# Optimization experiments

Measured on AMD Instinct MI355X. Metric: run time of the kernel, lower is better.

Reference implementation:

```python
import jax, jax.numpy as jnp
import numpy as np

FEAT_STRIDE = 16
PRE_N = 3000      # n_test_pre_nms
POST_N = 300      # n_test_post_nms
NMS_IOU = 0.7
MIN_SIZE = 16.0
SCALE = 1.0


def _anchor_base():
    base = 16.0
    ratios = np.array([0.5, 1.0, 2.0])
    scales = np.array([8.0, 16.0, 32.0])
    hs = (base * scales[None, :] * np.sqrt(ratios[:, None])).ravel()
    ws = (base * scales[None, :] * np.sqrt(1.0 / ratios[:, None])).ravel()
    px = py = base / 2.0
    return np.stack([px - ws / 2, py - hs / 2, px + ws / 2, py + hs / 2], axis=1).astype(np.float32)  # (9,4)


def _all_anchors(h, w):
    ab = _anchor_base()                                  # (A,4)
    sy = np.arange(h) * FEAT_STRIDE
    sx = np.arange(w) * FEAT_STRIDE
    yy, xx = np.meshgrid(sy, sx, indexing='ij')          # row-major (y,x) matches NHWC flatten
    shifts = np.stack([xx.ravel(), yy.ravel(), xx.ravel(), yy.ravel()], axis=1).astype(np.float32)
    return jnp.asarray((shifts[:, None, :] + ab[None, :, :]).reshape(-1, 4))  # (h*w*A, 4)


def _loc2box(anchor, loc):
    w = anchor[:, 2] - anchor[:, 0]
    h = anchor[:, 3] - anchor[:, 1]
    cx = anchor[:, 0] + 0.5 * w
    cy = anchor[:, 1] + 0.5 * h
    ctr_x = loc[:, 0] * w + cx
    ctr_y = loc[:, 1] * h + cy
    nw = jnp.exp(loc[:, 2]) * w
    nh = jnp.exp(loc[:, 3]) * h
    return jnp.stack([ctr_x - 0.5 * nw, ctr_y - 0.5 * nh, ctr_x + 0.5 * nw, ctr_y + 0.5 * nh], axis=1)


def _iou(b):
    area = (b[:, 2] - b[:, 0]) * (b[:, 3] - b[:, 1])
    x1 = jnp.maximum(b[:, None, 0], b[None, :, 0])
    y1 = jnp.maximum(b[:, None, 1], b[None, :, 1])
    x2 = jnp.minimum(b[:, None, 2], b[None, :, 2])
    y2 = jnp.minimum(b[:, None, 3], b[None, :, 3])
    inter = jnp.maximum(x2 - x1, 0.0) * jnp.maximum(y2 - y1, 0.0)
    return inter / (area[:, None] + area[None, :] - inter + 1e-9)


def _proposals(loc, score, anchor, img_h, img_w):
    roi = _loc2box(anchor, loc)
    roi = jnp.stack([jnp.clip(roi[:, 0], 0.0, img_w), jnp.clip(roi[:, 1], 0.0, img_h),
                     jnp.clip(roi[:, 2], 0.0, img_w), jnp.clip(roi[:, 3], 0.0, img_h)], axis=1)
    ms = MIN_SIZE * SCALE
    valid = ((roi[:, 2] - roi[:, 0]) >= ms) & ((roi[:, 3] - roi[:, 1]) >= ms)
    score = jnp.where(valid, score, -1e9)  # size filter as masking (jit-friendly)
    _, top_i = jax.lax.top_k(score, PRE_N)  # descending argsort + pre-NMS cut
    boxes = roi[top_i]                       # (PRE_N,4), score-sorted
    iou = _iou(boxes)
    idx = jnp.arange(PRE_N)

    def body(i, keep):
        sup = jnp.any(keep & (iou[i] > NMS_IOU) & (idx < i))
        return keep.at[i].set(~sup)

    keep = jax.lax.fori_loop(0, PRE_N, body, jnp.zeros((PRE_N,), bool))
    sel = jnp.sort(jnp.where(keep, idx, PRE_N))[:POST_N]
    sel = jnp.where(sel >= PRE_N, 0, sel)  # pad with top box (index 0 is always kept)
    return boxes[sel]                       # (POST_N,4)


def setup_inputs() -> dict:
    key = jax.random.key(0)
    ks = jax.random.split(key, 4)
    n, C, M, H, W, A = 4, 512, 512, 64, 64, 9
    x = jax.random.normal(ks[0], (n, C, H, W), jnp.float32)
    w_conv = jax.random.normal(ks[1], (M, C, 3, 3), jnp.float32) * 0.01
    b_conv = jnp.zeros((M,), jnp.float32)
    w_score = jax.random.normal(ks[2], (A * 2, M, 1, 1), jnp.float32) * 0.01
    b_score = jnp.zeros((A * 2,), jnp.float32)
    w_loc = jax.random.normal(ks[3], (A * 4, M, 1, 1), jnp.float32) * 0.01
    b_loc = jnp.zeros((A * 4,), jnp.float32)
    return dict(x=x, w_conv=w_conv, b_conv=b_conv, w_score=w_score, b_score=b_score,
                w_loc=w_loc, b_loc=b_loc, img_h=1024, img_w=1024)


def reference(x, w_conv, b_conv, w_score, b_score, w_loc, b_loc, img_h, img_w):
    n, _, h, w = x.shape
    dn = ('NCHW', 'OIHW', 'NCHW')
    feat = jax.nn.relu(jax.lax.conv_general_dilated(x, w_conv, (1, 1), 'SAME', dimension_numbers=dn)
                       + b_conv[None, :, None, None])
    rpn_locs = jax.lax.conv_general_dilated(feat, w_loc, (1, 1), 'SAME', dimension_numbers=dn) + b_loc[None, :, None, None]
    rpn_locs = rpn_locs.transpose(0, 2, 3, 1).reshape(n, -1, 4)
    rpn_scores = jax.lax.conv_general_dilated(feat, w_score, (1, 1), 'SAME', dimension_numbers=dn) + b_score[None, :, None, None]
    rpn_scores = rpn_scores.transpose(0, 2, 3, 1).reshape(n, -1, 2)
    fg = jax.nn.softmax(rpn_scores, axis=-1)[:, :, 1]  # (n, h*w*A)
    anchor = _all_anchors(h, w)
    rois = jax.vmap(lambda l, s: _proposals(l, s, anchor, float(img_h), float(img_w)))(rpn_locs, fg)
    roi_indices = jnp.repeat(jnp.arange(n, dtype=jnp.float32)[:, None], POST_N, axis=1)
    return rpn_locs, rpn_scores, rois, roi_indices, anchor[None]
```

## Files before the change

kernel.cpp:

```cpp
#include <hip/hip_runtime.h>
#include <cstdint>
#include <cmath>

#define HW 64
#define NPIX 4096
#define CIN 512
#define NANCH 36864
#define PREN 3000
#define POSTN 300
#define ICL 8
#define NSLOT 13

typedef _Float16 h8v __attribute__((ext_vector_type(8)));
typedef float f16v __attribute__((ext_vector_type(16)));

#define AS1 __attribute__((address_space(1)))
#define AS3 __attribute__((address_space(3)))

__device__ __forceinline__ void gl16(const void* g, void* l) {
  __builtin_amdgcn_global_load_lds((const AS1 void*)g, (AS3 void*)l, 16, 0, 0);
}

__device__ __forceinline__ void f16_split(float f, short& h, short& l) {
  _Float16 hh = (_Float16)f;
  float hf = (float)hh;
  _Float16 ll = (_Float16)(f - hf);
  h = __builtin_bit_cast(short, hh);
  l = __builtin_bit_cast(short, ll);
}


__global__ __launch_bounds__(256) void xform_w_kernel(
    const float* __restrict__ w, short* __restrict__ wth,
    short* __restrict__ wtl, unsigned* __restrict__ zp) {
  const int oc = blockIdx.x;
  const int t = threadIdx.x;
  __shared__ float ws_[4608];
  const float* wr = w + (size_t)oc * 4608;
  for (int i = t; i < 4608; i += 256) ws_[i] = wr[i];
  __syncthreads();
  for (int c = t; c < 576; c += 256) {
    int tap = c / 64;
    int g = c - tap * 64;
    int icc = g >> 2;
    int kh = (g >> 1) & 1;
    int lhh = g & 1;
    h8v hv, lv;
    short* hp = (short*)&hv;
    short* lp = (short*)&lv;
#pragma unroll
    for (int j = 0; j < 8; ++j) {
      short hh, ll;
      f16_split(ws_[(g * 8 + j) * 9 + tap] * 128.0f, hh, ll);
      hp[j] = hh; lp[j] = ll;
    }
    long o = (((((long)tap * 16 + icc) * 2 + kh) * 2 + lhh) * 512 + oc) * 8;
    *(h8v*)(wth + o) = hv;
    *(h8v*)(wtl + o) = lv;
  }
  if (oc == 0 && t < 16) zp[t] = 0u;
}

__global__ __launch_bounds__(256) void xform_x_kernel(
    const float* __restrict__ x, short* __restrict__ xth,
    short* __restrict__ xtl) {
  const int yb = blockIdx.x;
  const int n = blockIdx.y;
  const int t = threadIdx.x;
  __shared__ float xs[64 * 65];
  const float* xr = x + ((size_t)n * 512) * 4096 + yb * 64;
  short* oh = xth + ((size_t)n * 4096 + yb * 64) * 512;
  short* ol = xtl + ((size_t)n * 4096 + yb * 64) * 512;
  for (int icb = 0; icb < 8; ++icb) {
    if (icb) __syncthreads();
#pragma unroll
    for (int q = 0; q < 16; ++q) {
      int idx = q * 256 + t;
      int icl = idx >> 6, xc = idx & 63;
      xs[icl * 65 + xc] = xr[(size_t)(icb * 64 + icl) * 4096 + xc];
    }
    __syncthreads();
#pragma unroll
    for (int q = 0; q < 2; ++q) {
      int c = q * 256 + t;
      int xc = c >> 3, icg = c & 7;
      h8v hv, lv;
      short* hp = (short*)&hv;
      short* lp = (short*)&lv;
#pragma unroll
      for (int j = 0; j < 8; ++j) {
        short hh, ll;
        f16_split(xs[(icg * 8 + j) * 65 + xc] * 2048.0f, hh, ll);
        hp[j] = hh; lp[j] = ll;
      }
      size_t o = (size_t)xc * 512 + icb * 64 + icg * 8;
      *(h8v*)(oh + o) = hv;
      *(h8v*)(ol + o) = lv;
    }
  }
}

__global__ __launch_bounds__(256, 2) void conv3_mfma(
    const short* __restrict__ xth, const short* __restrict__ xtl,
    const short* __restrict__ wth, const short* __restrict__ wtl,
    const float* __restrict__ bconv, const char* __restrict__ zpage,
    float* __restrict__ feat2) {
  const int t = threadIdx.x;
  const int lane = t & 63;
  const int wid = __builtin_amdgcn_readfirstlane(t >> 6);
  const int l31 = lane & 31, lh = lane >> 5;
  const int wm = wid >> 1, wn = wid & 1;

  const int bx = blockIdx.x, by = blockIdx.y, n = blockIdx.z;
  const int k8 = bx & 7;
  const int ocb = k8 & 3;
  const int yp = (k8 >> 2) * 16 + (bx >> 3) * 4 + by;
  const int y0 = yp * 2;
  const int ocbase = ocb * 128;

  __shared__ short As[2][2][272 * 32];
  char* const asb = (char*)&As[0][0][0];

  const char* asrc[9]; int adst[9]; int astep[9];
  {
    const char* xs0 = (const char*)xth;
    const char* xs1 = (const char*)xtl;
#pragma unroll
    for (int k = 0; k < 9; ++k) {
      int bq = wid + 4 * k;
      if (bq < 34) {
        int hl = (bq >= 17) ? 1 : 0;
        int blk = bq - hl * 17;
        int e = blk * 16 + (lane >> 2);
        int slot = lane & 3;
        int r = e / 68;
        int cp = e - r * 68;
        int y = y0 - 1 + r;
        int c = cp - 1;
        bool valid = (cp >= 1) && (cp <= 64) && (y >= 0) && (y < 64);
        int ss = slot ^ ((e >> 1) & 3);
        long off = ((((long)n * 64 + y) * 64 + c) * 512 + ss * 8) * 2;
        asrc[k] = valid ? ((hl ? xs1 : xs0) + off) : (const char*)zpage;
        astep[k] = valid ? 64 : 0;
        adst[k] = hl * 17408 + blk * 1024;
      }
    }
  }

  const long lane_b = (long)lh * 4096 + (long)(ocbase + wn * 64 + l31) * 8;

  struct FragB { h8v h[2][2], l[2][2]; };

#define READ_Bg(F, TAP, ICC) do {                                            \
    long sb_ = ((long)(TAP) * 16 + (ICC)) * 16384 + lane_b;                  \
    _Pragma("unroll")                                                        \
    for (int kh_ = 0; kh_ < 2; ++kh_)                                        \
      _Pragma("unroll")                                                      \
      for (int fn_ = 0; fn_ < 2; ++fn_) {                                    \
        long o_ = sb_ + kh_ * 8192 + fn_ * 256;                              \
        (F).h[kh_][fn_] = *(const h8v*)(wth + o_);                           \
        (F).l[kh_][fn_] = *(const h8v*)(wtl + o_);                           \
      }                                                                      \
  } while (0)

#define COMP_AE(AE, TAP) do {                                                 \
    int dy_ = (TAP) / 3, dx_ = (TAP) - dy_ * 3;                               \
    _Pragma("unroll")                                                         \
    for (int fm_ = 0; fm_ < 2; ++fm_) {                                       \
      int e_ = (wm + dy_) * 68 + fm_ * 32 + l31 + dx_;                        \
      (AE)[fm_] = e_ * 64 + ((lh ^ ((e_ >> 1) & 3)) << 4);                    \
    }                                                                         \
  } while (0)

#define TAP_MFMA(BC, AB) do {                                                 \
    _Pragma("unroll")                                                         \
    for (int kh_ = 0; kh_ < 2; ++kh_) {                                       \
      h8v Ah_[2], Al_[2];                                                     \
      _Pragma("unroll")                                                       \
      for (int fm_ = 0; fm_ < 2; ++fm_) {                                     \
        int a0_ = ae[fm_] ^ (kh_ << 5);                                       \
        Ah_[fm_] = *(const h8v*)((AB) + a0_);                                 \
        Al_[fm_] = *(const h8v*)((AB) + 17408 + a0_);                         \
      }                                                                       \
      _Pragma("unroll")                                                       \
      for (int fm_ = 0; fm_ < 2; ++fm_)                                       \
        _Pragma("unroll")                                                     \
        for (int fn_ = 0; fn_ < 2; ++fn_)                                     \
          acc[fm_][fn_] = __builtin_amdgcn_mfma_f32_32x32x16_f16(             \
              Ah_[fm_], (BC).h[kh_][fn_], acc[fm_][fn_], 0, 0, 0);            \
      _Pragma("unroll")                                                       \
      for (int fm_ = 0; fm_ < 2; ++fm_)                                       \
        _Pragma("unroll")                                                     \
        for (int fn_ = 0; fn_ < 2; ++fn_)                                     \
          acc[fm_][fn_] = __builtin_amdgcn_mfma_f32_32x32x16_f16(             \
              Al_[fm_], (BC).h[kh_][fn_], acc[fm_][fn_], 0, 0, 0);            \
      _Pragma("unroll")                                                       \
      for (int fm_ = 0; fm_ < 2; ++fm_)                                       \
        _Pragma("unroll")                                                     \
        for (int fn_ = 0; fn_ < 2; ++fn_)                                     \
          acc[fm_][fn_] = __builtin_amdgcn_mfma_f32_32x32x16_f16(             \
              Ah_[fm_], (BC).l[kh_][fn_], acc[fm_][fn_], 0, 0, 0);            \
    }                                                                         \
  } while (0)

#define STEP_BODY(BC, BN) do {                                                \
    int tapN_ = tap + 1, iccN_ = icc;                                         \
    if (tapN_ == 9) { tapN_ = 0; iccN_ = (icc < 15) ? icc + 1 : 15; }         \
    READ_Bg(BN, tapN_, iccN_);             \
    if (tap == 0 && icc < 15) {            \
      char* ab_ = asb + ((acur ^ 1) * 34816);                                 \
      _Pragma("unroll")                                                       \
      for (int k_ = 0; k_ < 9; ++k_) {                                        \
        int bq_ = wid + 4 * k_;                                               \
        if (bq_ < 34) { asrc[k_] += astep[k_];                                \
                        gl16(asrc[k_], ab_ + adst[k_]); }                     \
      }                                                                       \
    }                                                                         \
    COMP_AE(ae, tap);                                                         \
    { char* abc_ = asb + (acur * 34816);                                      \
      TAP_MFMA(BC, abc_); }                                                   \
    ++tap;                                                                    \
    if (tap == 9) {                                         \
      tap = 0; ++icc;                                                         \
      _Pragma("unroll")                                                       \
      for (int fm_ = 0; fm_ < 2; ++fm_)                                       \
        _Pragma("unroll")                                                     \
        for (int fn_ = 0; fn_ < 2; ++fn_)                                     \
          _Pragma("unroll")                                                   \
          for (int r_ = 0; r_ < 16; ++r_) {                                   \
            S[fm_][fn_][r_] += acc[fm_][fn_][r_];                             \
            acc[fm_][fn_][r_] = 0.f;                                          \
          }                                                                   \
      __syncthreads();                      \
      acur ^= 1;                                                              \
    }                                                                         \
  } while (0)

  f16v acc[2][2];
  f16v S[2][2];
#pragma unroll
  for (int i = 0; i < 2; ++i)
#pragma unroll
    for (int j = 0; j < 2; ++j)
#pragma unroll
      for (int r = 0; r < 16; ++r) { acc[i][j][r] = 0.f; S[i][j][r] = 0.f; }

#pragma unroll
  for (int k = 0; k < 9; ++k) {
    int bq = wid + 4 * k;
    if (bq < 34) gl16(asrc[k], asb + adst[k]);
  }
  FragB B0, B1;
  READ_Bg(B0, 0, 0);
  __syncthreads();
  int ae[2];
  int tap = 0, icc = 0, acur = 0;

  for (int s2 = 0; s2 < 72; ++s2) {
    STEP_BODY(B0, B1);
    STEP_BODY(B1, B0);
  }

#undef READ_Bg
#undef COMP_AE
#undef TAP_MFMA
#undef STEP_BODY

  const float OS = 1.0f / 262144.0f;
  const float* bb = bconv + ocbase + wn * 64;
#pragma unroll
  for (int fn = 0; fn < 2; ++fn) {
    const float bias = bb[fn * 32 + l31];
#pragma unroll
    for (int fm = 0; fm < 2; ++fm) {
      float* op = feat2 + (((long)n * 4096 + (y0 + wm) * 64 + fm * 32) * 512)
                + ocbase + wn * 64 + fn * 32 + l31;
#pragma unroll
      for (int r = 0; r < 16; ++r) {
        int m = (r & 3) + 8 * (r >> 2) + 4 * lh;
        op[(long)m * 512] = fmaxf(S[fm][fn][r] * OS + bias, 0.f);
      }
    }
  }
}

__global__ __launch_bounds__(256) void zero_hist_kernel(unsigned* __restrict__ h) {
  int i = blockIdx.x * 256 + threadIdx.x;
  if (i < 262160) h[i] = 0u;
}

__global__ __launch_bounds__(256) void reshape_w_kernel(
    const float* __restrict__ w, float* __restrict__ w4,
    unsigned* __restrict__ histz) {
  int gid = blockIdx.x * 256 + threadIdx.x;
  if (gid < 262160) histz[gid] = 0;
  if (gid >= 512 * 512 * 9) return;
  int o4  = gid & 3;
  int r   = gid >> 2;
  int tap = r % 9;
  int r2  = r / 9;
  int h   = r2 & 1;
  int r3  = r2 >> 1;
  int ic  = r3 & 511;
  int g   = r3 >> 9;
  int oc  = (g >> 2) * 32 + (g & 3) * 8 + h * 4 + o4;
  w4[gid] = w[((size_t)oc * 512 + ic) * 9 + tap];
}

#define WLOAD(DST, UPTR) do {                                                \
    _Pragma("unroll")                                                        \
    for (int q = 0; q < 36; ++q) (DST)[q] = (UPTR)[q];                       \
  } while (0)

#define CONV_HALF(W, OB) do {                                                \
    _Pragma("unroll")                                                        \
    for (int r = 0; r < 3; ++r)                                              \
    _Pragma("unroll")                                                        \
    for (int kx = 0; kx < 3; ++kx) {                                         \
      _Pragma("unroll")                                                      \
      for (int o = 0; o < 4; ++o) {                                          \
        const float wv = (W)[(r * 3 + kx) * 4 + o];                          \
        _Pragma("unroll")                                                    \
        for (int j = 0; j < 4; ++j)                                          \
          acc[(OB) + o][j] = fmaf(wv, xr[r][j + kx], acc[(OB) + o][j]);      \
      }                                                                      \
    }                                                                        \
  } while (0)

__global__ __launch_bounds__(256, 4) void conv3_kernel(
    const float* __restrict__ x, const float* __restrict__ w4,
    const float* __restrict__ b, float* __restrict__ feat2) {
  const int oct = blockIdx.x;
  const int yt  = blockIdx.y;
  const int n   = blockIdx.z;
  const int t   = threadIdx.x;
  const int wid  = __builtin_amdgcn_readfirstlane(t >> 6);
  const int lane = t & 63;
  const int lrow = lane >> 4;
  const int lcol = (lane & 15) << 2;
  const int y0 = yt << 2;

  __shared__ float xs[2][ICL * 6 * 68];

  float acc[8][4];
#pragma unroll
  for (int o = 0; o < 8; ++o)
#pragma unroll
    for (int j = 0; j < 4; ++j) acc[o][j] = 0.f;

  const float* xb = x + (size_t)n * CIN * NPIX;
  const float* __restrict__ wq = w4 + (size_t)(oct * 4 + wid) * (512 * 72);

  int  goff[NSLOT];
  int  laddr[NSLOT];
  bool val[NSLOT];
#pragma unroll
  for (int k = 0; k < NSLOT; ++k) {
    int s   = t + (k << 8);
    int icl = s / 396;
    int rem = s - icl * 396;
    int row = rem / 66;
    int c   = rem - row * 66;
    int yy = y0 - 1 + row;
    int xx = c - 1;
    bool act = (k < NSLOT - 1) || (t < 96);
    val[k]  = act && ((unsigned)yy < 64u) && ((unsigned)xx < 64u);
    goff[k] = icl * NPIX + yy * 64 + xx;
    laddr[k] = icl * 408 + row * 68 + c;
  }

  {
    float v[NSLOT];
#pragma unroll
    for (int k = 0; k < NSLOT; ++k) v[k] = val[k] ? xb[goff[k]] : 0.f;
#pragma unroll
    for (int k = 0; k < NSLOT; ++k)
      if (k < NSLOT - 1 || t < 96) xs[0][laddr[k]] = v[k];
  }

  float wbA[36], wbB[36];
  WLOAD(wbA, wq);

  for (int cch = 0; cch < 64; ++cch) {
    const int cur = cch & 1;
    float rn[NSLOT];
    if (cch < 63) {
      const float* xn = xb + (size_t)(cch + 1) * (ICL * NPIX);
#pragma unroll
      for (int k = 0; k < NSLOT; ++k) rn[k] = val[k] ? xn[goff[k]] : 0.f;
    }
    __syncthreads();
#pragma unroll 1
    for (int icl = 0; icl < ICL; ++icl) {
      const int u0 = (cch << 4) + (icl << 1);
      const float* xp = &xs[cur][icl * 408 + lrow * 68 + lcol];
      float4 a0 = *(const float4*)(xp);
      float2 b0 = *(const float2*)(xp + 4);
      float4 a1 = *(const float4*)(xp + 68);
      float2 b1 = *(const float2*)(xp + 72);
      float4 a2 = *(const float4*)(xp + 136);
      float2 b2 = *(const float2*)(xp + 140);
      float xr[3][6] = {{a0.x, a0.y, a0.z, a0.w, b0.x, b0.y},
                        {a1.x, a1.y, a1.z, a1.w, b1.x, b1.y},
                        {a2.x, a2.y, a2.z, a2.w, b2.x, b2.y}};
      WLOAD(wbB, wq + (size_t)(u0 + 1) * 36);
      CONV_HALF(wbA, 0);
      {
        const int un = (u0 + 2 < 1024) ? (u0 + 2) : 1023;
        WLOAD(wbA, wq + (size_t)un * 36);
      }
      CONV_HALF(wbB, 4);
    }
    if (cch < 63) {
#pragma unroll
      for (int k = 0; k < NSLOT; ++k)
        if (k < NSLOT - 1 || t < 96) xs[cur ^ 1][laddr[k]] = rn[k];
    }
  }

  const float* __restrict__ bs = b + oct * 32 + wid * 8;
  float bias[8];
#pragma unroll
  for (int o = 0; o < 8; ++o) bias[o] = bs[o];
  float* ob = feat2 + ((size_t)n * NPIX + (y0 + lrow) * 64 + lcol) * 512 + oct * 32 + wid * 8;
#pragma unroll
  for (int j = 0; j < 4; ++j) {
    float4 v0, v1;
    v0.x = fmaxf(acc[0][j] + bias[0], 0.f);
    v0.y = fmaxf(acc[1][j] + bias[1], 0.f);
    v0.z = fmaxf(acc[2][j] + bias[2], 0.f);
    v0.w = fmaxf(acc[3][j] + bias[3], 0.f);
    v1.x = fmaxf(acc[4][j] + bias[4], 0.f);
    v1.y = fmaxf(acc[5][j] + bias[5], 0.f);
    v1.z = fmaxf(acc[6][j] + bias[6], 0.f);
    v1.w = fmaxf(acc[7][j] + bias[7], 0.f);
    *(float4*)(ob + (size_t)j * 512)     = v0;
    *(float4*)(ob + (size_t)j * 512 + 4) = v1;
  }
}

__global__ __launch_bounds__(256) void conv1_decode_kernel(
    const float* __restrict__ feat2,
    const float* __restrict__ w_loc, const float* __restrict__ b_loc,
    const float* __restrict__ w_score, const float* __restrict__ b_score,
    const int* __restrict__ ih, const int* __restrict__ iw,
    float* __restrict__ out_locs, float* __restrict__ out_scores,
    float* __restrict__ boxes, unsigned* __restrict__ keys,
    unsigned* __restrict__ hist, float* __restrict__ out_anchor) {
#pragma clang fp contract(off)
  const int y  = blockIdx.x, n = blockIdx.y, hf = blockIdx.z;
  const int t = threadIdx.x;
  const int lane = t & 63;
  const int pg = t >> 4;
  const int cg = t & 15;
  __shared__ float fl2[128 * 34];
  __shared__ float wl2[128 * 64];
  float acc[2][4];
#pragma unroll
  for (int i = 0; i < 2; ++i)
#pragma unroll
    for (int j = 0; j < 4; ++j) acc[i][j] = 0.f;

  const float* fb = feat2 + ((size_t)n * NPIX + y * 64 + hf * 32) * 512;
  for (int ch = 0; ch < 512; ch += 128) {
    for (int idx = t; idx < 32 * 128; idx += 256) {
      int p = idx >> 7, ic = idx & 127;
      fl2[ic * 34 + p] = fb[(size_t)p * 512 + ch + ic];
    }
    for (int idx = t; idx < 64 * 128; idx += 256) {
      int c = idx & 63, ic = idx >> 6;
      float v = 0.f;
      if (c < 36) v = w_loc[c * 512 + ch + ic];
      else if (c < 54) v = w_score[(c - 36) * 512 + ch + ic];
      wl2[ic * 64 + c] = v;
    }
    __syncthreads();
#pragma unroll 4
    for (int ic = 0; ic < 128; ++ic) {
      float2 f = *(const float2*)&fl2[ic * 34 + pg * 2];
      float4 w = *(const float4*)&wl2[ic * 64 + cg * 4];
      float fv[2] = {f.x, f.y};
      float wv[4] = {w.x, w.y, w.z, w.w};
#pragma unroll
      for (int i = 0; i < 2; ++i)
#pragma unroll
        for (int j = 0; j < 4; ++j)
          acc[i][j] = fmaf(wv[j], fv[i], acc[i][j]);
    }
    __syncthreads();
  }
#pragma unroll
  for (int j = 0; j < 4; ++j) {
    int c = cg * 4 + j;
    float bias = (c < 36) ? b_loc[c] : (c < 54 ? b_score[c - 36] : 0.f);
#pragma unroll
    for (int i = 0; i < 2; ++i) {
      int pxl = pg * 2 + i;
      float v = acc[i][j] + bias;
      size_t pix0 = (size_t)y * 64 + hf * 32 + pxl;
      if (c < 36) {
        out_locs[((size_t)n * NPIX + pix0) * 36 + c] = v;
        fl2[pxl * 56 + c] = v;
      } else if (c < 54) {
        out_scores[((size_t)n * NPIX + pix0) * 18 + (c - 36)] = v;
        fl2[pxl * 56 + c] = v;
      }
    }
  }
  __syncthreads();
  for (int task = t; task < 288; task += 256) {
    int lpx = task / 9;
    int a   = task - lpx * 9;
    int xq = hf * 32 + lpx, yq = y;
    int i = (yq * 64 + xq) * 9 + a;
    int gid = n * NANCH + i;
    int ri = a / 3, si = a - ri * 3;
    double ratio = (ri == 0) ? 0.5 : (ri == 1 ? 1.0 : 2.0);
    double scl   = (si == 0) ? 8.0 : (si == 1 ? 16.0 : 32.0);
    double hh = 16.0 * scl * sqrt(ratio);
    double ww = 16.0 * scl * sqrt(1.0 / ratio);
    float sx = (float)(xq * 16), sy = (float)(yq * 16);
    float ax1 = (float)(8.0 - ww * 0.5) + sx;
    float ay1 = (float)(8.0 - hh * 0.5) + sy;
    float ax2 = (float)(8.0 + ww * 0.5) + sx;
    float ay2 = (float)(8.0 + hh * 0.5) + sy;
    if (n == 0) {
      *(float4*)(out_anchor + (size_t)i * 4) = make_float4(ax1, ay1, ax2, ay2);
    }
    float l0 = fl2[lpx * 56 + a * 4 + 0];
    float l1 = fl2[lpx * 56 + a * 4 + 1];
    float l2 = fl2[lpx * 56 + a * 4 + 2];
    float l3 = fl2[lpx * 56 + a * 4 + 3];
    float aw = ax2 - ax1, ah = ay2 - ay1;
    float cx = ax1 + 0.5f * aw, cy = ay1 + 0.5f * ah;
    float ctrx = l0 * aw + cx, ctry = l1 * ah + cy;
    float nw = expf(l2) * aw, nh = expf(l3) * ah;
    float x1 = ctrx - 0.5f * nw, y1 = ctry - 0.5f * nh;
    float x2 = ctrx + 0.5f * nw, y2 = ctry + 0.5f * nh;
    float W = (float)iw[0], H = (float)ih[0];
    x1 = fminf(fmaxf(x1, 0.f), W);
    y1 = fminf(fmaxf(y1, 0.f), H);
    x2 = fminf(fmaxf(x2, 0.f), W);
    y2 = fminf(fmaxf(y2, 0.f), H);
    bool valid = ((x2 - x1) >= 16.f) && ((y2 - y1) >= 16.f);
    float s0 = fl2[lpx * 56 + 36 + a * 2];
    float s1 = fl2[lpx * 56 + 36 + a * 2 + 1];
    float mx = fmaxf(s0, s1);
    float e0 = expf(s0 - mx), e1 = expf(s1 - mx);
    float fg = e1 / (e0 + e1);
    float sc = valid ? fg : -1e9f;
    unsigned bb = __float_as_uint(sc);
    unsigned v = (bb & 0x80000000u) ? ~bb : (bb | 0x80000000u);
    keys[gid] = v;
    *(float4*)(boxes + (size_t)gid * 4) = make_float4(x1, y1, x2, y2);
    unsigned bin = v >> 16;
    unsigned tix = ((bin & 255u) << 8) | (bin >> 8);
    unsigned long long mv = __ballot(!valid);
    if (!valid) {
      int leader = __ffsll(mv) - 1;
      if (lane == leader)
        atomicAdd(&hist[(size_t)n * 65536 + tix], (unsigned)__popcll(mv));
    } else {
      atomicAdd(&hist[(size_t)n * 65536 + tix], 1u);
    }
  }
}

__global__ __launch_bounds__(256) void compact_kernel(
    const unsigned* __restrict__ keys, const unsigned* __restrict__ hist,
    unsigned* __restrict__ cnt, unsigned long long* __restrict__ cand) {
  int t = threadIdx.x;
  int gid = blockIdx.x * 256 + t;
  int lane = t & 63;
  int n = (blockIdx.x << 8) / NANCH;
  int i = gid - n * NANCH;
  const unsigned* h = hist + (size_t)n * 65536;
  __shared__ unsigned csum[256];
  __shared__ unsigned fine[256];
  __shared__ unsigned csel, cumsh, cutsh;
  unsigned s = 0;
  for (int low = 0; low < 256; ++low) s += h[low * 256 + t];
  csum[t] = s;
  __syncthreads();
  if (t == 0) {
    unsigned cum = 0;
    int c = 255;
    for (; c > 0; --c) {
      if (cum + csum[c] >= PREN) break;
      cum += csum[c];
    }
    csel = (unsigned)c;
    cumsh = cum;
  }
  __syncthreads();
  int c = (int)csel;
  fine[t] = h[t * 256 + c];
  __syncthreads();
  if (t == 0) {
    unsigned cum = cumsh;
    unsigned P = (unsigned)(c << 8);
    for (int low = 255; low >= 0; --low) {
      cum += fine[low];
      if (cum >= PREN) { P = (unsigned)((c << 8) | low); break; }
    }
    cutsh = P;
  }
  __syncthreads();
  unsigned P = cutsh;
  unsigned v = keys[gid];
  bool take = (v >> 16) >= P;
  unsigned long long m = __ballot(take);
  if (take) {
    int leader = __ffsll(m) - 1;
    int tot = __popcll(m);
    int pre = __popcll(m & ((lane == 0) ? 0ull : (~0ull >> (64 - lane))));
    unsigned base = 0;
    if (lane == leader) base = atomicAdd(&cnt[n], (unsigned)tot);
    base = __shfl(base, leader);
    cand[(size_t)n * NANCH + base + pre] =
        ((unsigned long long)v << 32) | (unsigned)(~i);
  }
}

__global__ __launch_bounds__(256) void rank2_kernel(
    const unsigned long long* __restrict__ cand, const unsigned* __restrict__ cnt,
    const float* __restrict__ boxes, float* __restrict__ sboxes) {
  int n = blockIdx.y;
  int C = (int)cnt[n];
  if (blockIdx.x * 256 >= C) return;
  int t = threadIdx.x;
  int i = blockIdx.x * 256 + t;
  const unsigned long long* cb = cand + (size_t)n * NANCH;
  unsigned long long Ki = (i < C) ? cb[i] : 0ull;
  __shared__ unsigned long long tile[256];
  int rank = 0;
  for (int t0 = 0; t0 < C; t0 += 256) {
    __syncthreads();
    int j = t0 + t;
    tile[t] = (j < C) ? cb[j] : 0ull;
    __syncthreads();
#pragma unroll 16
    for (int jj = 0; jj < 256; ++jj)
      rank += (tile[jj] > Ki) ? 1 : 0;
  }
  if (i < C && rank < PREN) {
    unsigned orig = ~(unsigned)(Ki & 0xffffffffull);
    float4 bb = *(const float4*)(boxes + ((size_t)n * NANCH + orig) * 4);
    *(float4*)(sboxes + ((size_t)n * PREN + rank) * 4) = bb;
  }
}

__global__ __launch_bounds__(256) void iou_kernel(
    const float* __restrict__ sboxes, unsigned long long* __restrict__ sup) {
#pragma clang fp contract(off)
  int n = blockIdx.y, i = blockIdx.x;
  const float* B = sboxes + (size_t)n * PREN * 4;
  float4 bi = *(const float4*)(B + (size_t)i * 4);
  float area_i = (bi.z - bi.x) * (bi.w - bi.y);
  int lane = threadIdx.x & 63, wv = threadIdx.x >> 6;
  unsigned long long* row = sup + ((size_t)n * PREN + i) * 64;
  for (int w0 = wv; w0 < 64; w0 += 4) {
    int j = w0 * 64 + lane;
    bool p = false;
    if (j < PREN) {
      float4 bj = *(const float4*)(B + (size_t)j * 4);
      float area_j = (bj.z - bj.x) * (bj.w - bj.y);
      float x1 = fmaxf(bi.x, bj.x), y1 = fmaxf(bi.y, bj.y);
      float x2 = fminf(bi.z, bj.z), y2 = fminf(bi.w, bj.w);
      float inter = fmaxf(x2 - x1, 0.f) * fmaxf(y2 - y1, 0.f);
      float iou = inter / (area_i + area_j - inter + 1e-9f);
      p = iou > 0.7f;
    }
    unsigned long long m = __ballot(p);
    if (lane == 0) row[w0] = m;
  }
}

__global__ __launch_bounds__(64) void nms_kernel(
    const unsigned long long* __restrict__ sup, const float* __restrict__ sboxes,
    float* __restrict__ rois, float* __restrict__ ridx) {
  int n = blockIdx.x;
  int lane = threadIdx.x;
  const unsigned long long* S = sup + (size_t)n * PREN * 64;
  unsigned long long buf[64];
#pragma unroll
  for (int bq = 0; bq < 64; ++bq) buf[bq] = S[(size_t)bq * 64 + lane];
  unsigned long long keep = (lane < 46) ? ~0ull
                          : (lane == 46 ? ((1ull << 56) - 1ull) : 0ull);
  int tot = 0;
  for (int w = 0; w < 47; ++w) {
    unsigned long long rw[64];
#pragma unroll
    for (int bq = 0; bq < 64; ++bq) rw[bq] = __shfl(buf[bq], w);
    unsigned long long kw = __shfl(keep, w);
#pragma unroll
    for (int bq = 0; bq < 64; ++bq) {
      unsigned long long amask = ((kw >> bq) & 1ull) ? ~0ull : 0ull;
      const unsigned long long fmask = (bq == 63) ? 0ull : ~((2ull << bq) - 1ull);
      kw &= ~(rw[bq] & fmask & amask);
    }
    unsigned long long gmask = (lane > w) ? ~0ull : 0ull;
#pragma unroll
    for (int bq = 0; bq < 64; ++bq) {
      unsigned long long amask = ((kw >> bq) & 1ull) ? ~0ull : 0ull;
      keep &= ~(buf[bq] & gmask & amask);
      const int i = w * 64 + bq;
      if (i + 64 < PREN) buf[bq] = S[(size_t)(i + 64) * 64 + lane];
    }
    keep = (lane == w) ? kw : keep;
    tot += __popcll(kw);
    if (tot >= POSTN) {
      if (lane > w) keep = 0ull;
      break;
    }
  }
  int cnt = __popcll(keep);
  int scn = cnt;
  for (int d = 1; d < 64; d <<= 1) {
    int v = __shfl_up(scn, d);
    if (lane >= d) scn += v;
  }
  int excl = scn - cnt;
  int total = __shfl(scn, 63);
  const float* SB = sboxes + (size_t)n * PREN * 4;
  unsigned long long kk = keep;
  int p = excl;
  while (kk) {
    int bpos = __ffsll(kk) - 1;
    kk &= kk - 1ull;
    if (p < POSTN) {
      float4 bb = *(const float4*)(SB + (size_t)(lane * 64 + bpos) * 4);
      *(float4*)(rois + ((size_t)n * POSTN + p) * 4) = bb;
    }
    ++p;
  }
  if (lane == 0) {
    float4 b0 = *(const float4*)SB;
    for (int q = total; q < POSTN; ++q)
      *(float4*)(rois + ((size_t)n * POSTN + q) * 4) = b0;
  }
  for (int q = lane; q < POSTN; q += 64) ridx[n * POSTN + q] = (float)n;
}

extern "C" void kernel_launch(void* const* d_in, const int* in_sizes, int n_in,
                              void* d_out, int out_size, void* d_ws, size_t ws_size,
                              hipStream_t stream) {
  const float* x       = (const float*)d_in[0];
  const float* w_conv  = (const float*)d_in[1];
  const float* b_conv  = (const float*)d_in[2];
  const float* w_score = (const float*)d_in[3];
  const float* b_score = (const float*)d_in[4];
  const float* w_loc   = (const float*)d_in[5];
  const float* b_loc   = (const float*)d_in[6];
  const int*   img_h   = (const int*)d_in[7];
  const int*   img_w   = (const int*)d_in[8];

  float* out        = (float*)d_out;
  float* out_locs   = out;
  float* out_scores = out + 589824;
  float* out_rois   = out + 884736;
  float* out_ridx   = out + 889536;
  float* out_anchor = out + 890736;

  const size_t NEED = 76546112;
  if (ws_size >= NEED) {
    float* feat2 = (float*)d_ws;
    short* wth   = (short*)((char*)d_ws + 33554432);
    short* wtl   = wth + 2359296;
    short* xth   = (short*)((char*)d_ws + 42991616);
    short* xtl   = xth + 8388608;
    char*  zpage = (char*)d_ws + 76546048;
    float* boxes = (float*)wth;
    unsigned* keys = (unsigned*)(boxes + 589824);
    float* sboxes  = (float*)(keys + 147456);
    unsigned long long* sup = (unsigned long long*)(sboxes + 48000);
    unsigned* hist = (unsigned*)xth;
    unsigned* cnt  = hist + 262148;
    unsigned long long* cand = (unsigned long long*)(hist + 262160);

    xform_w_kernel<<<512, 256, 0, stream>>>(w_conv, wth, wtl, (unsigned*)zpage);
    xform_x_kernel<<<dim3(64, 4), 256, 0, stream>>>(x, xth, xtl);
    conv3_mfma<<<dim3(32, 4, 4), 256, 0, stream>>>(xth, xtl, wth, wtl, b_conv,
                                                   zpage, feat2);
    zero_hist_kernel<<<1025, 256, 0, stream>>>(hist);
    conv1_decode_kernel<<<dim3(64, 4, 2), 256, 0, stream>>>(
        feat2, w_loc, b_loc, w_score, b_score, img_h, img_w,
        out_locs, out_scores, boxes, keys, hist, out_anchor);
    compact_kernel<<<576, 256, 0, stream>>>(keys, hist, cnt, cand);
    rank2_kernel<<<dim3(144, 4), 256, 0, stream>>>(cand, cnt, boxes, sboxes);
    iou_kernel<<<dim3(PREN, 4), 256, 0, stream>>>(sboxes, sup);
    nms_kernel<<<4, 64, 0, stream>>>(sup, sboxes, out_rois, out_ridx);
  } else {
    float* feat2 = (float*)d_ws;
    float* A     = feat2 + (size_t)8388608;
    float* w4    = A;
    float* boxes = A;
    unsigned* keys = (unsigned*)(boxes + 589824);
    float* sboxes  = (float*)(keys + 147456);
    unsigned long long* sup = (unsigned long long*)(sboxes + 48000);
    unsigned* hist = (unsigned*)(A + 2359296);
    unsigned* cnt  = hist + 262148;
    unsigned long long* cand = (unsigned long long*)(hist + 262160);

    reshape_w_kernel<<<9216, 256, 0, stream>>>(w_conv, w4, hist);
    conv3_kernel<<<dim3(16, 16, 4), 256, 0, stream>>>(x, w4, b_conv, feat2);
    conv1_decode_kernel<<<dim3(64, 4, 2), 256, 0, stream>>>(
        feat2, w_loc, b_loc, w_score, b_score, img_h, img_w,
        out_locs, out_scores, boxes, keys, hist, out_anchor);
    compact_kernel<<<576, 256, 0, stream>>>(keys, hist, cnt, cand);
    rank2_kernel<<<dim3(144, 4), 256, 0, stream>>>(cand, cnt, boxes, sboxes);
    iou_kernel<<<dim3(PREN, 4), 256, 0, stream>>>(sboxes, sup);
    nms_kernel<<<4, 64, 0, stream>>>(sup, sboxes, out_rois, out_ridx);
  }
}
```

Before: 577.0 us.

## Pre-transpose 1x1 conv weights and split decode kernel into finer pixel blocks

Adds a small kernel that writes the loc and score 1x1 weights once into a transposed [ic][64] layout in workspace. The decode kernel then reads those weights straight from global or cache instead of restaging them in LDS for every block. Each block now covers 16 pixels instead of 32, so twice as many blocks run, with one pixel and four channels per thread. This removes the redundant weight gather and shrinks LDS use to raise occupancy, at the cost of more global weight loads per FMA and an extra kernel launch.

```diff
diff --git a/kernel.cpp b/kernel.cpp
--- a/kernel.cpp
+++ b/kernel.cpp
@@ -98,6 +98,18 @@
       *(h8v*)(ol + o) = lv;
     }
   }
+}
+
+__global__ __launch_bounds__(256) void xform_w1_kernel(
+    const float* __restrict__ w_loc, const float* __restrict__ w_score,
+    float* __restrict__ w1t) {
+  int i = blockIdx.x * 256 + threadIdx.x;
+  if (i >= 32768) return;
+  int ic = i >> 6, oc = i & 63;
+  float v = 0.f;
+  if (oc < 36) v = w_loc[oc * 512 + ic];
+  else if (oc < 54) v = w_score[(oc - 36) * 512 + ic];
+  w1t[i] = v;
 }
 
 __global__ __launch_bounds__(256, 2) void conv3_mfma(
@@ -440,9 +452,8 @@
 }
 
 __global__ __launch_bounds__(256) void conv1_decode_kernel(
-    const float* __restrict__ feat2,
-    const float* __restrict__ w_loc, const float* __restrict__ b_loc,
-    const float* __restrict__ w_score, const float* __restrict__ b_score,
+    const float* __restrict__ feat2, const float* __restrict__ w1t,
+    const float* __restrict__ b_loc, const float* __restrict__ b_score,
     const int* __restrict__ ih, const int* __restrict__ iw,
     float* __restrict__ out_locs, float* __restrict__ out_scores,
     float* __restrict__ boxes, unsigned* __restrict__ keys,
@@ -453,65 +464,49 @@
   const int lane = t & 63;
   const int pg = t >> 4;
   const int cg = t & 15;
-  __shared__ float fl2[128 * 34];
-  __shared__ float wl2[128 * 64];
-  float acc[2][4];
-#pragma unroll
-  for (int i = 0; i < 2; ++i)
-#pragma unroll
-    for (int j = 0; j < 4; ++j) acc[i][j] = 0.f;
-
-  const float* fb = feat2 + ((size_t)n * NPIX + y * 64 + hf * 32) * 512;
+  __shared__ float fl2[128 * 19];
+  float acc[4];
+  acc[0] = acc[1] = acc[2] = acc[3] = 0.f;
+
+  const float* fb = feat2 + ((size_t)n * NPIX + y * 64 + hf * 16) * 512;
   for (int ch = 0; ch < 512; ch += 128) {
-    for (int idx = t; idx < 32 * 128; idx += 256) {
+    if (ch) __syncthreads();
+    for (int idx = t; idx < 16 * 128; idx += 256) {
       int p = idx >> 7, ic = idx & 127;
-      fl2[ic * 34 + p] = fb[(size_t)p * 512 + ch + ic];
-    }
-    for (int idx = t; idx < 64 * 128; idx += 256) {
-      int c = idx & 63, ic = idx >> 6;
-      float v = 0.f;
-      if (c < 36) v = w_loc[c * 512 + ch + ic];
-      else if (c < 54) v = w_score[(c - 36) * 512 + ch + ic];
-      wl2[ic * 64 + c] = v;
+      fl2[ic * 19 + p] = fb[(size_t)p * 512 + ch + ic];
     }
     __syncthreads();
 #pragma unroll 4
     for (int ic = 0; ic < 128; ++ic) {
-      float2 f = *(const float2*)&fl2[ic * 34 + pg * 2];
-      float4 w = *(const float4*)&wl2[ic * 64 + cg * 4];
-      float fv[2] = {f.x, f.y};
-      float wv[4] = {w.x, w.y, w.z, w.w};
-#pragma unroll
-      for (int i = 0; i < 2; ++i)
-#pragma unroll
-        for (int j = 0; j < 4; ++j)
-          acc[i][j] = fmaf(wv[j], fv[i], acc[i][j]);
-    }
-    __syncthreads();
-  }
+      float f = fl2[ic * 19 + pg];
+      float4 w = *(const float4*)&w1t[(size_t)(ch + ic) * 64 + cg * 4];
+      acc[0] = fmaf(w.x, f, acc[0]);
+      acc[1] = fmaf(w.y, f, acc[1]);
+      acc[2] = fmaf(w.z, f, acc[2]);
+      acc[3] = fmaf(w.w, f, acc[3]);
+    }
+  }
+  __syncthreads();
 #pragma unroll
   for (int j = 0; j < 4; ++j) {
     int c = cg * 4 + j;
     float bias = (c < 36) ? b_loc[c] : (c < 54 ? b_score[c - 36] : 0.f);
-#pragma unroll
-    for (int i = 0; i < 2; ++i) {
-      int pxl = pg * 2 + i;
-      float v = acc[i][j] + bias;
-      size_t pix0 = (size_t)y * 64 + hf * 32 + pxl;
-      if (c < 36) {
-        out_locs[((size_t)n * NPIX + pix0) * 36 + c] = v;
-        fl2[pxl * 56 + c] = v;
-      } else if (c < 54) {
-        out_scores[((size_t)n * NPIX + pix0) * 18 + (c - 36)] = v;
-        fl2[pxl * 56 + c] = v;
-      }
+    int pxl = pg;
+    float v = acc[j] + bias;
+    size_t pix0 = (size_t)y * 64 + hf * 16 + pxl;
+    if (c < 36) {
+      out_locs[((size_t)n * NPIX + pix0) * 36 + c] = v;
+      fl2[pxl * 56 + c] = v;
+    } else if (c < 54) {
+      out_scores[((size_t)n * NPIX + pix0) * 18 + (c - 36)] = v;
+      fl2[pxl * 56 + c] = v;
     }
   }
   __syncthreads();
-  for (int task = t; task < 288; task += 256) {
+  for (int task = t; task < 144; task += 256) {
     int lpx = task / 9;
     int a   = task - lpx * 9;
-    int xq = hf * 32 + lpx, yq = y;
+    int xq = hf * 16 + lpx, yq = y;
     int i = (yq * 64 + xq) * 9 + a;
     int gid = n * NANCH + i;
     int ri = a / 3, si = a - ri * 3;
@@ -777,14 +772,16 @@
     unsigned* hist = (unsigned*)xth;
     unsigned* cnt  = hist + 262148;
     unsigned long long* cand = (unsigned long long*)(hist + 262160);
+    float* w1t = (float*)((char*)d_ws + 47185920);
 
     xform_w_kernel<<<512, 256, 0, stream>>>(w_conv, wth, wtl, (unsigned*)zpage);
     xform_x_kernel<<<dim3(64, 4), 256, 0, stream>>>(x, xth, xtl);
     conv3_mfma<<<dim3(32, 4, 4), 256, 0, stream>>>(xth, xtl, wth, wtl, b_conv,
                                                    zpage, feat2);
     zero_hist_kernel<<<1025, 256, 0, stream>>>(hist);
-    conv1_decode_kernel<<<dim3(64, 4, 2), 256, 0, stream>>>(
-        feat2, w_loc, b_loc, w_score, b_score, img_h, img_w,
+    xform_w1_kernel<<<128, 256, 0, stream>>>(w_loc, w_score, w1t);
+    conv1_decode_kernel<<<dim3(64, 4, 4), 256, 0, stream>>>(
+        feat2, w1t, b_loc, b_score, img_h, img_w,
         out_locs, out_scores, boxes, keys, hist, out_anchor);
     compact_kernel<<<576, 256, 0, stream>>>(keys, hist, cnt, cand);
     rank2_kernel<<<dim3(144, 4), 256, 0, stream>>>(cand, cnt, boxes, sboxes);
@@ -801,11 +798,13 @@
     unsigned* hist = (unsigned*)(A + 2359296);
     unsigned* cnt  = hist + 262148;
     unsigned long long* cand = (unsigned long long*)(hist + 262160);
+    float* w1t = (float*)(cand + 147456);
 
     reshape_w_kernel<<<9216, 256, 0, stream>>>(w_conv, w4, hist);
+    xform_w1_kernel<<<128, 256, 0, stream>>>(w_loc, w_score, w1t);
     conv3_kernel<<<dim3(16, 16, 4), 256, 0, stream>>>(x, w4, b_conv, feat2);
-    conv1_decode_kernel<<<dim3(64, 4, 2), 256, 0, stream>>>(
-        feat2, w_loc, b_loc, w_score, b_score, img_h, img_w,
+    conv1_decode_kernel<<<dim3(64, 4, 4), 256, 0, stream>>>(
+        feat2, w1t, b_loc, b_score, img_h, img_w,
         out_locs, out_scores, boxes, keys, hist, out_anchor);
     compact_kernel<<<576, 256, 0, stream>>>(keys, hist, cnt, cand);
     rank2_kernel<<<dim3(144, 4), 256, 0, stream>>>(cand, cnt, boxes, sboxes);
```

Measured after the change: 588.7 us. 1.02x slower.
